# Kernel tuning notes

Hardware: AMD Instinct MI355X
Metric: run time of the kernel (lower is better)

## Reference

```python
import jax, jax.numpy as jnp
import numpy as np

N_NODES = 100000
DIM_IN = 128
DIM_OUT = 128
N_EDGES = 1600000
EPS = 0.0  # PyG GINConv default, non-trainable


def setup_inputs() -> dict:
    key = jax.random.key(0)
    k1, k2, k3, k4, k5, k6 = jax.random.split(key, 6)
    node_feature = jax.random.normal(k1, (N_NODES, DIM_IN), dtype=jnp.float32)
    edge_index = jax.random.randint(k2, (2, N_EDGES), 0, N_NODES, dtype=jnp.int64)
    s1 = 1.0 / np.sqrt(DIM_IN)
    s2 = 1.0 / np.sqrt(DIM_OUT)
    W1 = jax.random.uniform(k3, (DIM_IN, DIM_OUT), jnp.float32, -s1, s1)
    b1 = jax.random.uniform(k4, (DIM_OUT,), jnp.float32, -s1, s1)
    W2 = jax.random.uniform(k5, (DIM_OUT, DIM_OUT), jnp.float32, -s2, s2)
    b2 = jax.random.uniform(k6, (DIM_OUT,), jnp.float32, -s2, s2)
    return {"node_feature": node_feature, "edge_index": edge_index,
            "W1": W1, "b1": b1, "W2": W2, "b2": b2}


def reference(node_feature, edge_index, W1, b1, W2, b2):
    src, dst = edge_index[0], edge_index[1]
    # scatter-add neighbor aggregation: messages x_j = x[src] summed at dst
    agg = jax.ops.segment_sum(node_feature[src], dst, num_segments=N_NODES)  # [N, d]
    h = (1.0 + EPS) * node_feature + agg
    h = jax.nn.relu(h @ W1 + b1)
    return h @ W2 + b2
```

## Files before the change

kernel.cpp:

```cpp
#include <hip/hip_runtime.h>

#define NN 100000
#define D  128
#define NE 1600000

#define NBK2 782
#define CAP2 2816
#define EPB  8192
#define NFB  196
#define ENTCAP 2048

typedef __bf16 bf16x8 __attribute__((ext_vector_type(8)));
typedef __bf16 bf16x4 __attribute__((ext_vector_type(4)));
typedef float  f32x4  __attribute__((ext_vector_type(4)));

__global__ void xprep_kernel(const float* __restrict__ x, __bf16* __restrict__ xb) {
    int i = blockIdx.x * 256 + threadIdx.x;
    if (i < NN * 32) {
        float4 v = reinterpret_cast<const float4*>(x)[i];
        bf16x4 o = {(__bf16)v.x, (__bf16)v.y, (__bf16)v.z, (__bf16)v.w};
        reinterpret_cast<bf16x4*>(xb)[i] = o;
    }
}

__global__ void wprep_kernel(const float* __restrict__ W1, const float* __restrict__ W2,
                             __bf16* __restrict__ w1t, __bf16* __restrict__ w2t) {
    int i = blockIdx.x * 256 + threadIdx.x;
    if (i < 16384) {
        int c = i >> 7, k = i & 127;
        w1t[i] = (__bf16)W1[k * 128 + c];
    } else if (i < 32768) {
        int j = i - 16384;
        int c = j >> 7, k = j & 127;
        w2t[j] = (__bf16)W2[k * 128 + c];
    }
}

__global__ void zero_gcur_kernel(int* __restrict__ gcur) {
    int i = blockIdx.x * 256 + threadIdx.x;
    if (i < NBK2) gcur[i] = 0;
}

__global__ __launch_bounds__(512)
void fill2_kernel(const int* __restrict__ ei, int* __restrict__ gcur,
                  int* __restrict__ bedge) {
    __shared__ int            stage[EPB];
    __shared__ unsigned short bid16[EPB];
    __shared__ int            lofs[NBK2];
    __shared__ int            lpos[NBK2];
    __shared__ int            gbase[NBK2];
    __shared__ int            ssum[512];
    __shared__ int            tot;

    const int tid = threadIdx.x;
    const int e0  = blockIdx.x * EPB;

    for (int b = tid; b < NBK2; b += 512) lpos[b] = 0;
    __syncthreads();

    int eb[16], epk[16];
    #pragma unroll 16
    for (int k = 0; k < 16; ++k) {
        int e = e0 + k * 512 + tid;
        eb[k] = -1;
        if (e < NE) {
            int s = ei[e];
            int d = ei[NE + e];
            if ((unsigned)s < NN && (unsigned)d < NN) {
                eb[k]  = d >> 7;
                epk[k] = ((d & 127) << 17) | s;
                atomicAdd(&lpos[eb[k]], 1);
            }
        }
    }
    __syncthreads();

    int t2 = tid * 2;
    int c0 = (t2 < NBK2) ? lpos[t2] : 0;
    int c1 = (t2 + 1 < NBK2) ? lpos[t2 + 1] : 0;
    ssum[tid] = c0 + c1;
    __syncthreads();
    for (int off = 1; off < 512; off <<= 1) {
        int v = (tid >= off) ? ssum[tid - off] : 0;
        __syncthreads();
        ssum[tid] += v;
        __syncthreads();
    }
    int excl = ssum[tid] - (c0 + c1);
    if (t2 < NBK2) {
        lofs[t2] = excl;
        lpos[t2] = excl;
        if (c0) gbase[t2] = atomicAdd(&gcur[t2], c0);
    }
    if (t2 + 1 < NBK2) {
        lofs[t2 + 1] = excl + c0;
        lpos[t2 + 1] = excl + c0;
        if (c1) gbase[t2 + 1] = atomicAdd(&gcur[t2 + 1], c1);
    }
    if (tid == 511) tot = ssum[511];
    __syncthreads();

    #pragma unroll 16
    for (int k = 0; k < 16; ++k) {
        if (eb[k] >= 0) {
            int r = atomicAdd(&lpos[eb[k]], 1);
            stage[r] = epk[k];
            bid16[r] = (unsigned short)eb[k];
        }
    }
    __syncthreads();

    int T = tot;
    for (int i = tid; i < T; i += 512) {
        int b   = bid16[i];
        int pos = gbase[b] + (i - lofs[b]);
        if (pos < CAP2) bedge[b * CAP2 + pos] = stage[i];
    }
}

__global__ __launch_bounds__(256)
void gather3_kernel(const __bf16* __restrict__ xb, const int* __restrict__ gcur,
                    const int* __restrict__ bedge, __bf16* __restrict__ hb) {
    __shared__ int ent[ENTCAP];
    __shared__ int c64[64], ofs[65], cur[64], scn[64];

    const int b    = blockIdx.x >> 1;
    const int half = blockIdx.x & 1;
    const int tid  = threadIdx.x;

    int cnt = gcur[b]; if (cnt > CAP2) cnt = CAP2;
    const int base = b * CAP2;

    if (tid < 64) c64[tid] = 0;
    __syncthreads();

    for (int i = tid; i < cnt; i += 256) {
        int v  = bedge[base + i];
        int dl = v >> 17;
        if ((dl >> 6) == half) atomicAdd(&c64[dl & 63], 1);
    }
    __syncthreads();

    if (tid < 64) scn[tid] = c64[tid];
    __syncthreads();
    #pragma unroll
    for (int off = 1; off < 64; off <<= 1) {
        int v = (tid >= off && tid < 64) ? scn[tid - off] : 0;
        __syncthreads();
        if (tid < 64) scn[tid] += v;
        __syncthreads();
    }
    if (tid < 64) {
        ofs[tid + 1] = scn[tid];
        if (tid == 0) ofs[0] = 0;
        cur[tid] = scn[tid] - c64[tid];
    }
    __syncthreads();

    for (int i = tid; i < cnt; i += 256) {
        int v  = bedge[base + i];
        int dl = v >> 17;
        if ((dl >> 6) == half) {
            int r = atomicAdd(&cur[dl & 63], 1);
            if (r < ENTCAP) ent[r] = v & 0x1FFFF;
        }
    }
    __syncthreads();

    const int wave   = tid >> 6;
    const int lane   = tid & 63;
    const int half32 = lane >> 5;
    const int l31    = lane & 31;
    const bf16x4* xv4 = reinterpret_cast<const bf16x4*>(xb);

    for (int q = wave; q < 64; q += 4) {
        int node = b * 128 + half * 64 + q;
        if (node >= NN) continue;
        int beg = ofs[q], end = ofs[q + 1];
        if (beg > ENTCAP) beg = ENTCAP;
        if (end > ENTCAP) end = ENTCAP;

        float a0 = 0.f, a1 = 0.f, a2 = 0.f, a3 = 0.f;
        float b0 = 0.f, b1 = 0.f, b2f = 0.f, b3 = 0.f;
        int j = beg;
        for (; j + 4 <= end; j += 4) {
            int s0 = ent[j + half32];
            int s1 = ent[j + 2 + half32];
            bf16x4 v0 = xv4[(size_t)s0 * 32 + l31];
            bf16x4 v1 = xv4[(size_t)s1 * 32 + l31];
            a0 += (float)v0[0]; a1 += (float)v0[1];
            a2 += (float)v0[2]; a3 += (float)v0[3];
            b0 += (float)v1[0]; b1 += (float)v1[1];
            b2f += (float)v1[2]; b3 += (float)v1[3];
        }
        if (j + 2 <= end) {
            int s0 = ent[j + half32];
            bf16x4 v0 = xv4[(size_t)s0 * 32 + l31];
            a0 += (float)v0[0]; a1 += (float)v0[1];
            a2 += (float)v0[2]; a3 += (float)v0[3];
            j += 2;
        }
        if (j < end && half32 == 0) {
            int s0 = ent[j];
            bf16x4 v0 = xv4[(size_t)s0 * 32 + l31];
            a0 += (float)v0[0]; a1 += (float)v0[1];
            a2 += (float)v0[2]; a3 += (float)v0[3];
        }
        a0 += b0; a1 += b1; a2 += b2f; a3 += b3;
        a0 += __shfl_xor(a0, 32); a1 += __shfl_xor(a1, 32);
        a2 += __shfl_xor(a2, 32); a3 += __shfl_xor(a3, 32);

        if (half32 == 0) {
            bf16x4 sv = xv4[(size_t)node * 32 + l31];
            bf16x4 o = {(__bf16)(a0 + (float)sv[0]), (__bf16)(a1 + (float)sv[1]),
                        (__bf16)(a2 + (float)sv[2]), (__bf16)(a3 + (float)sv[3])};
            reinterpret_cast<bf16x4*>(hb)[(size_t)node * 32 + l31] = o;
        }
    }
}

__global__ __launch_bounds__(256)
void mlp_mfma_kernel(const __bf16* __restrict__ hb,
                     const __bf16* __restrict__ w1t,
                     const __bf16* __restrict__ w2t,
                     const float* __restrict__ b1,
                     const float* __restrict__ b2,
                     float* __restrict__ out) {
    __shared__ __align__(16) unsigned char sh_h[64 * 256];
    __shared__ __align__(16) unsigned char sh_w[128 * 256];

    const int tid   = threadIdx.x;
    const int wv    = tid >> 6;
    const int lane  = tid & 63;
    const int l15   = lane & 15;
    const int kbyte = (lane >> 4) * 16;
    const int row0  = blockIdx.x * 64;

    for (int c = tid; c < 1024; c += 256) {
        int r = c >> 4, s = c & 15;
        int grow = row0 + r;
        int4 val = make_int4(0, 0, 0, 0);
        if (grow < NN) val = *reinterpret_cast<const int4*>(hb + (size_t)grow * 128 + s * 8);
        *reinterpret_cast<int4*>(sh_h + r * 256 + ((s * 16) ^ ((r & 7) << 4))) = val;
    }
    for (int c = tid; c < 2048; c += 256) {
        int r = c >> 4, s = c & 15;
        int4 val = *reinterpret_cast<const int4*>(w1t + r * 128 + s * 8);
        *reinterpret_cast<int4*>(sh_w + r * 256 + ((s * 16) ^ ((r & 7) << 4))) = val;
    }
    __syncthreads();

    bf16x8 bf1[2][4];
    #pragma unroll
    for (int nn = 0; nn < 2; ++nn) {
        int col = wv * 32 + nn * 16 + l15;
        #pragma unroll
        for (int ks = 0; ks < 4; ++ks)
            bf1[nn][ks] = *reinterpret_cast<const bf16x8*>(
                sh_w + col * 256 + ((ks * 64 + kbyte) ^ ((col & 7) << 4)));
    }

    f32x4 acc[4][2];
    #pragma unroll
    for (int m = 0; m < 4; ++m) {
        acc[m][0] = f32x4{0.f, 0.f, 0.f, 0.f};
        acc[m][1] = f32x4{0.f, 0.f, 0.f, 0.f};
        int row = m * 16 + l15;
        bf16x8 af[4];
        #pragma unroll
        for (int ks = 0; ks < 4; ++ks)
            af[ks] = *reinterpret_cast<const bf16x8*>(
                sh_h + row * 256 + ((ks * 64 + kbyte) ^ ((row & 7) << 4)));
        #pragma unroll
        for (int ks = 0; ks < 4; ++ks) {
            acc[m][0] = __builtin_amdgcn_mfma_f32_16x16x32_bf16(af[ks], bf1[0][ks], acc[m][0], 0, 0, 0);
            acc[m][1] = __builtin_amdgcn_mfma_f32_16x16x32_bf16(af[ks], bf1[1][ks], acc[m][1], 0, 0, 0);
        }
    }

    float bias1a = b1[wv * 32 + l15];
    float bias1b = b1[wv * 32 + 16 + l15];

    __syncthreads();

    #pragma unroll
    for (int m = 0; m < 4; ++m) {
        #pragma unroll
        for (int nn = 0; nn < 2; ++nn) {
            int col = wv * 32 + nn * 16 + l15;
            float bb = nn ? bias1b : bias1a;
            #pragma unroll
            for (int j = 0; j < 4; ++j) {
                int row = m * 16 + (lane >> 4) * 4 + j;
                float v = fmaxf(acc[m][nn][j] + bb, 0.f);
                *reinterpret_cast<__bf16*>(
                    sh_h + row * 256 + ((col * 2) ^ ((row & 7) << 4))) = (__bf16)v;
            }
        }
    }
    for (int c = tid; c < 2048; c += 256) {
        int r = c >> 4, s = c & 15;
        int4 val = *reinterpret_cast<const int4*>(w2t + r * 128 + s * 8);
        *reinterpret_cast<int4*>(sh_w + r * 256 + ((s * 16) ^ ((r & 7) << 4))) = val;
    }
    __syncthreads();

    bf16x8 bf2[2][4];
    #pragma unroll
    for (int nn = 0; nn < 2; ++nn) {
        int col = wv * 32 + nn * 16 + l15;
        #pragma unroll
        for (int ks = 0; ks < 4; ++ks)
            bf2[nn][ks] = *reinterpret_cast<const bf16x8*>(
                sh_w + col * 256 + ((ks * 64 + kbyte) ^ ((col & 7) << 4)));
    }

    f32x4 acc2[4][2];
    #pragma unroll
    for (int m = 0; m < 4; ++m) {
        acc2[m][0] = f32x4{0.f, 0.f, 0.f, 0.f};
        acc2[m][1] = f32x4{0.f, 0.f, 0.f, 0.f};
        int row = m * 16 + l15;
        bf16x8 af[4];
        #pragma unroll
        for (int ks = 0; ks < 4; ++ks)
            af[ks] = *reinterpret_cast<const bf16x8*>(
                sh_h + row * 256 + ((ks * 64 + kbyte) ^ ((row & 7) << 4)));
        #pragma unroll
        for (int ks = 0; ks < 4; ++ks) {
            acc2[m][0] = __builtin_amdgcn_mfma_f32_16x16x32_bf16(af[ks], bf2[0][ks], acc2[m][0], 0, 0, 0);
            acc2[m][1] = __builtin_amdgcn_mfma_f32_16x16x32_bf16(af[ks], bf2[1][ks], acc2[m][1], 0, 0, 0);
        }
    }

    float bias2a = b2[wv * 32 + l15];
    float bias2b = b2[wv * 32 + 16 + l15];
    #pragma unroll
    for (int m = 0; m < 4; ++m) {
        #pragma unroll
        for (int nn = 0; nn < 2; ++nn) {
            int col = wv * 32 + nn * 16 + l15;
            float bb = nn ? bias2b : bias2a;
            #pragma unroll
            for (int j = 0; j < 4; ++j) {
                int row = row0 + m * 16 + (lane >> 4) * 4 + j;
                if (row < NN) out[(size_t)row * 128 + col] = acc2[m][nn][j] + bb;
            }
        }
    }
}

extern "C" void kernel_launch(void* const* d_in, const int* in_sizes, int n_in,
                              void* d_out, int out_size, void* d_ws, size_t ws_size,
                              hipStream_t stream) {
    const float* x  = (const float*)d_in[0];
    const int*   ei = (const int*)d_in[1];
    const float* W1 = (const float*)d_in[2];
    const float* b1 = (const float*)d_in[3];
    const float* W2 = (const float*)d_in[4];
    const float* b2 = (const float*)d_in[5];
    float* out = (float*)d_out;

    int* gcur  = (int*)d_ws;
    int* bedge = gcur + NBK2;
    size_t int_end = (size_t)(NBK2 + (size_t)NBK2 * CAP2) * 4;
    size_t bf_off  = (int_end + 255) & ~(size_t)255;
    __bf16* xb  = (__bf16*)((char*)d_ws + bf_off);
    __bf16* hb  = xb + (size_t)NN * D;
    __bf16* w1t = hb + (size_t)NN * D;
    __bf16* w2t = w1t + D * D;

    xprep_kernel<<<(NN * 32 + 255) / 256, 256, 0, stream>>>(x, xb);
    wprep_kernel<<<128, 256, 0, stream>>>(W1, W2, w1t, w2t);
    zero_gcur_kernel<<<(NBK2 + 255) / 256, 256, 0, stream>>>(gcur);

    fill2_kernel<<<NFB, 512, 0, stream>>>(ei, gcur, bedge);
    gather3_kernel<<<NBK2 * 2, 256, 0, stream>>>(xb, gcur, bedge, hb);

    mlp_mfma_kernel<<<(NN + 63) / 64, 256, 0, stream>>>(hb, w1t, w2t, b1, b2, out);
}
```

Before: 134.9 us.

## Merge prep kernels, halve fill block size, restructure MLP to 128-row blocks

Three prep launches (x to bf16, weight transpose, counter zeroing) are merged into one kernel keyed by block index, which saves launch gaps. The fill kernel now handles 4096 edges per block across 391 blocks to spread the work over more CUs. The MLP kernel handles 128 rows per block with 8 waves and reads weight fragments directly from global memory instead of staging them in LDS, which cuts LDS use and barriers but relies on cache hits for the weight reads.

```diff
diff --git a/kernel.cpp b/kernel.cpp
--- a/kernel.cpp
+++ b/kernel.cpp
@@ -6,39 +6,45 @@
 
 #define NBK2 782
 #define CAP2 2816
-#define EPB  8192
-#define NFB  196
+#define EPB  4096
+#define NFB  391
 #define ENTCAP 2048
+
+#define PREP_XB   12500
+#define PREP_W    128
+#define PREP_Z    4
+#define PREP_GRID (PREP_XB + PREP_W + PREP_Z)
 
 typedef __bf16 bf16x8 __attribute__((ext_vector_type(8)));
 typedef __bf16 bf16x4 __attribute__((ext_vector_type(4)));
 typedef float  f32x4  __attribute__((ext_vector_type(4)));
 
-__global__ void xprep_kernel(const float* __restrict__ x, __bf16* __restrict__ xb) {
-    int i = blockIdx.x * 256 + threadIdx.x;
-    if (i < NN * 32) {
+__global__ __launch_bounds__(256)
+void prep_kernel(const float* __restrict__ x, const float* __restrict__ W1,
+                 const float* __restrict__ W2, __bf16* __restrict__ xb,
+                 __bf16* __restrict__ w1t, __bf16* __restrict__ w2t,
+                 int* __restrict__ gcur) {
+    const int bid = blockIdx.x;
+    const int tid = threadIdx.x;
+    if (bid < PREP_XB) {
+        int i = bid * 256 + tid;
         float4 v = reinterpret_cast<const float4*>(x)[i];
         bf16x4 o = {(__bf16)v.x, (__bf16)v.y, (__bf16)v.z, (__bf16)v.w};
         reinterpret_cast<bf16x4*>(xb)[i] = o;
-    }
-}
-
-__global__ void wprep_kernel(const float* __restrict__ W1, const float* __restrict__ W2,
-                             __bf16* __restrict__ w1t, __bf16* __restrict__ w2t) {
-    int i = blockIdx.x * 256 + threadIdx.x;
-    if (i < 16384) {
-        int c = i >> 7, k = i & 127;
-        w1t[i] = (__bf16)W1[k * 128 + c];
-    } else if (i < 32768) {
-        int j = i - 16384;
-        int c = j >> 7, k = j & 127;
-        w2t[j] = (__bf16)W2[k * 128 + c];
-    }
-}
-
-__global__ void zero_gcur_kernel(int* __restrict__ gcur) {
-    int i = blockIdx.x * 256 + threadIdx.x;
-    if (i < NBK2) gcur[i] = 0;
+    } else if (bid < PREP_XB + PREP_W) {
+        int i = (bid - PREP_XB) * 256 + tid;
+        if (i < 16384) {
+            int c = i >> 7, k = i & 127;
+            w1t[i] = (__bf16)W1[k * 128 + c];
+        } else {
+            int j = i - 16384;
+            int c = j >> 7, k = j & 127;
+            w2t[j] = (__bf16)W2[k * 128 + c];
+        }
+    } else {
+        int i = (bid - PREP_XB - PREP_W) * 256 + tid;
+        if (i < NBK2) gcur[i] = 0;
+    }
 }
 
 __global__ __launch_bounds__(512)
@@ -58,9 +64,9 @@
     for (int b = tid; b < NBK2; b += 512) lpos[b] = 0;
     __syncthreads();
 
-    int eb[16], epk[16];
-    #pragma unroll 16
-    for (int k = 0; k < 16; ++k) {
+    int eb[8], epk[8];
+    #pragma unroll 8
+    for (int k = 0; k < 8; ++k) {
         int e = e0 + k * 512 + tid;
         eb[k] = -1;
         if (e < NE) {
@@ -100,8 +106,8 @@
     if (tid == 511) tot = ssum[511];
     __syncthreads();
 
-    #pragma unroll 16
-    for (int k = 0; k < 16; ++k) {
+    #pragma unroll 8
+    for (int k = 0; k < 8; ++k) {
         if (eb[k] >= 0) {
             int r = atomicAdd(&lpos[eb[k]], 1);
             stage[r] = epk[k];
@@ -219,45 +225,43 @@
     }
 }
 
-__global__ __launch_bounds__(256)
-void mlp_mfma_kernel(const __bf16* __restrict__ hb,
-                     const __bf16* __restrict__ w1t,
-                     const __bf16* __restrict__ w2t,
-                     const float* __restrict__ b1,
-                     const float* __restrict__ b2,
-                     float* __restrict__ out) {
-    __shared__ __align__(16) unsigned char sh_h[64 * 256];
-    __shared__ __align__(16) unsigned char sh_w[128 * 256];
-
-    const int tid   = threadIdx.x;
-    const int wv    = tid >> 6;
-    const int lane  = tid & 63;
-    const int l15   = lane & 15;
-    const int kbyte = (lane >> 4) * 16;
-    const int row0  = blockIdx.x * 64;
-
-    for (int c = tid; c < 1024; c += 256) {
+__global__ __launch_bounds__(512)
+void mlp2_kernel(const __bf16* __restrict__ hb,
+                 const __bf16* __restrict__ w1t,
+                 const __bf16* __restrict__ w2t,
+                 const float* __restrict__ b1,
+                 const float* __restrict__ b2,
+                 float* __restrict__ out) {
+    __shared__ __align__(16) unsigned char sh_h[128 * 256];
+
+    const int tid  = threadIdx.x;
+    const int row0 = blockIdx.x * 128;
+
+    for (int c = tid; c < 2048; c += 512) {
         int r = c >> 4, s = c & 15;
         int grow = row0 + r;
         int4 val = make_int4(0, 0, 0, 0);
         if (grow < NN) val = *reinterpret_cast<const int4*>(hb + (size_t)grow * 128 + s * 8);
         *reinterpret_cast<int4*>(sh_h + r * 256 + ((s * 16) ^ ((r & 7) << 4))) = val;
     }
-    for (int c = tid; c < 2048; c += 256) {
-        int r = c >> 4, s = c & 15;
-        int4 val = *reinterpret_cast<const int4*>(w1t + r * 128 + s * 8);
-        *reinterpret_cast<int4*>(sh_w + r * 256 + ((s * 16) ^ ((r & 7) << 4))) = val;
-    }
-    __syncthreads();
-
-    bf16x8 bf1[2][4];
+    __syncthreads();
+
+    const int wave  = tid >> 6;
+    const int lane  = tid & 63;
+    const int wr    = wave >> 2;
+    const int wc    = wave & 3;
+    const int l15   = lane & 15;
+    const int kbyte = (lane >> 4) * 16;
+    const int kelem = (lane >> 4) * 8;
+
+    bf16x8 bf[2][4];
     #pragma unroll
     for (int nn = 0; nn < 2; ++nn) {
-        int col = wv * 32 + nn * 16 + l15;
+        int col = wc * 32 + nn * 16 + l15;
         #pragma unroll
         for (int ks = 0; ks < 4; ++ks)
-            bf1[nn][ks] = *reinterpret_cast<const bf16x8*>(
-                sh_w + col * 256 + ((ks * 64 + kbyte) ^ ((col & 7) << 4)));
+            bf[nn][ks] = *reinterpret_cast<const bf16x8*>(
+                w1t + col * 128 + ks * 32 + kelem);
     }
 
     f32x4 acc[4][2];
@@ -265,7 +269,7 @@
     for (int m = 0; m < 4; ++m) {
         acc[m][0] = f32x4{0.f, 0.f, 0.f, 0.f};
         acc[m][1] = f32x4{0.f, 0.f, 0.f, 0.f};
-        int row = m * 16 + l15;
+        int row = wr * 64 + m * 16 + l15;
         bf16x8 af[4];
         #pragma unroll
         for (int ks = 0; ks < 4; ++ks)
@@ -273,13 +277,13 @@
                 sh_h + row * 256 + ((ks * 64 + kbyte) ^ ((row & 7) << 4)));
         #pragma unroll
         for (int ks = 0; ks < 4; ++ks) {
-            acc[m][0] = __builtin_amdgcn_mfma_f32_16x16x32_bf16(af[ks], bf1[0][ks], acc[m][0], 0, 0, 0);
-            acc[m][1] = __builtin_amdgcn_mfma_f32_16x16x32_bf16(af[ks], bf1[1][ks], acc[m][1], 0, 0, 0);
-        }
-    }
-
-    float bias1a = b1[wv * 32 + l15];
-    float bias1b = b1[wv * 32 + 16 + l15];
+            acc[m][0] = __builtin_amdgcn_mfma_f32_16x16x32_bf16(af[ks], bf[0][ks], acc[m][0], 0, 0, 0);
+            acc[m][1] = __builtin_amdgcn_mfma_f32_16x16x32_bf16(af[ks], bf[1][ks], acc[m][1], 0, 0, 0);
+        }
+    }
+
+    float bias1a = b1[wc * 32 + l15];
+    float bias1b = b1[wc * 32 + 16 + l15];
 
     __syncthreads();
 
@@ -287,32 +291,26 @@
     for (int m = 0; m < 4; ++m) {
         #pragma unroll
         for (int nn = 0; nn < 2; ++nn) {
-            int col = wv * 32 + nn * 16 + l15;
+            int col = wc * 32 + nn * 16 + l15;
             float bb = nn ? bias1b : bias1a;
             #pragma unroll
             for (int j = 0; j < 4; ++j) {
-                int row = m * 16 + (lane >> 4) * 4 + j;
+                int row = wr * 64 + m * 16 + (lane >> 4) * 4 + j;
                 float v = fmaxf(acc[m][nn][j] + bb, 0.f);
                 *reinterpret_cast<__bf16*>(
                     sh_h + row * 256 + ((col * 2) ^ ((row & 7) << 4))) = (__bf16)v;
             }
         }
     }
-    for (int c = tid; c < 2048; c += 256) {
-        int r = c >> 4, s = c & 15;
-        int4 val = *reinterpret_cast<const int4*>(w2t + r * 128 + s * 8);
-        *reinterpret_cast<int4*>(sh_w + r * 256 + ((s * 16) ^ ((r & 7) << 4))) = val;
-    }
-    __syncthreads();
-
-    bf16x8 bf2[2][4];
+    __syncthreads();
+
     #pragma unroll
     for (int nn = 0; nn < 2; ++nn) {
-        int col = wv * 32 + nn * 16 + l15;
+        int col = wc * 32 + nn * 16 + l15;
         #pragma unroll
         for (int ks = 0; ks < 4; ++ks)
-            bf2[nn][ks] = *reinterpret_cast<const bf16x8*>(
-                sh_w + col * 256 + ((ks * 64 + kbyte) ^ ((col & 7) << 4)));
+            bf[nn][ks] = *reinterpret_cast<const bf16x8*>(
+                w2t + col * 128 + ks * 32 + kelem);
     }
 
     f32x4 acc2[4][2];
@@ -320,7 +318,7 @@
     for (int m = 0; m < 4; ++m) {
         acc2[m][0] = f32x4{0.f, 0.f, 0.f, 0.f};
         acc2[m][1] = f32x4{0.f, 0.f, 0.f, 0.f};
-        int row = m * 16 + l15;
+        int row = wr * 64 + m * 16 + l15;
         bf16x8 af[4];
         #pragma unroll
         for (int ks = 0; ks < 4; ++ks)
@@ -328,22 +326,22 @@
                 sh_h + row * 256 + ((ks * 64 + kbyte) ^ ((row & 7) << 4)));
         #pragma unroll
         for (int ks = 0; ks < 4; ++ks) {
-            acc2[m][0] = __builtin_amdgcn_mfma_f32_16x16x32_bf16(af[ks], bf2[0][ks], acc2[m][0], 0, 0, 0);
-            acc2[m][1] = __builtin_amdgcn_mfma_f32_16x16x32_bf16(af[ks], bf2[1][ks], acc2[m][1], 0, 0, 0);
-        }
-    }
-
-    float bias2a = b2[wv * 32 + l15];
-    float bias2b = b2[wv * 32 + 16 + l15];
+            acc2[m][0] = __builtin_amdgcn_mfma_f32_16x16x32_bf16(af[ks], bf[0][ks], acc2[m][0], 0, 0, 0);
+            acc2[m][1] = __builtin_amdgcn_mfma_f32_16x16x32_bf16(af[ks], bf[1][ks], acc2[m][1], 0, 0, 0);
+        }
+    }
+
+    float bias2a = b2[wc * 32 + l15];
+    float bias2b = b2[wc * 32 + 16 + l15];
     #pragma unroll
     for (int m = 0; m < 4; ++m) {
         #pragma unroll
         for (int nn = 0; nn < 2; ++nn) {
-            int col = wv * 32 + nn * 16 + l15;
+            int col = wc * 32 + nn * 16 + l15;
             float bb = nn ? bias2b : bias2a;
             #pragma unroll
             for (int j = 0; j < 4; ++j) {
-                int row = row0 + m * 16 + (lane >> 4) * 4 + j;
+                int row = row0 + wr * 64 + m * 16 + (lane >> 4) * 4 + j;
                 if (row < NN) out[(size_t)row * 128 + col] = acc2[m][nn][j] + bb;
             }
         }
@@ -370,12 +368,8 @@
     __bf16* w1t = hb + (size_t)NN * D;
     __bf16* w2t = w1t + D * D;
 
-    xprep_kernel<<<(NN * 32 + 255) / 256, 256, 0, stream>>>(x, xb);
-    wprep_kernel<<<128, 256, 0, stream>>>(W1, W2, w1t, w2t);
-    zero_gcur_kernel<<<(NBK2 + 255) / 256, 256, 0, stream>>>(gcur);
-
+    prep_kernel<<<PREP_GRID, 256, 0, stream>>>(x, W1, W2, xb, w1t, w2t, gcur);
     fill2_kernel<<<NFB, 512, 0, stream>>>(ei, gcur, bedge);
     gather3_kernel<<<NBK2 * 2, 256, 0, stream>>>(xb, gcur, bedge, hb);
-
-    mlp_mfma_kernel<<<(NN + 63) / 64, 256, 0, stream>>>(hb, w1t, w2t, b1, b2, out);
-}
+    mlp2_kernel<<<NBK2, 512, 0, stream>>>(hb, w1t, w2t, b1, b2, out);
+}
```

Result: slower. 140.5 us (+4.1%).
